# Optimization experiments

Measured on AMD Instinct MI355X. Metric: run time of the kernel, lower is better.

Reference implementation:

```python
import jax, jax.numpy as jnp
from jax import lax
import numpy as np

T, B, I, H, F, KEEP = 1000, 512, 64, 64, 128, 5
ALPHA = 20.0 / 100.0  # dt / tau


def setup_inputs() -> dict:
    key = jax.random.key(0)
    ks = jax.random.split(key, 9)
    s = 1.0 / np.sqrt(H)
    return {
        "x": jax.random.normal(ks[0], (T, B, I), jnp.float32),
        "h0": jnp.zeros((B, H), jnp.float32),
        "W_in": jax.random.normal(ks[1], (H, I), jnp.float32) * s,
        "b_in": jax.random.normal(ks[2], (H,), jnp.float32) * s,
        "W_hh": jax.random.normal(ks[3], (H, H), jnp.float32) * s,
        "b_hh": jax.random.normal(ks[4], (H,), jnp.float32) * s,
        "W1": jax.random.normal(ks[5], (F, KEEP * H), jnp.float32) / np.sqrt(KEEP * H),
        "b1": jax.random.normal(ks[6], (F,), jnp.float32) * 0.01,
        "W2": jax.random.normal(ks[7], (H, F), jnp.float32) / np.sqrt(F),
        "b2": jax.random.normal(ks[8], (H,), jnp.float32) * 0.01,
    }


def reference(x, h0, W_in, b_in, W_hh, b_hh, W1, b1, W2, b2):
    # CT-RNN with leaky integration; feedback via MLP on the last 5 hiddens
    # once 5 steps have accumulated. KC = 0.5*I, so the feedback mix is
    # h = 0.5*h_obs + 0.5*h_mlp.
    Tn, Bn, _ = x.shape
    Hn = h0.shape[1]
    buf0 = jnp.zeros((KEEP, Bn, Hn), x.dtype)  # oldest-first ring of hiddens

    def step(carry, inp):
        h, buf = carry
        xt, i = inp
        h_obs = jax.nn.relu(xt @ W_in.T + b_in + h @ W_hh.T + b_hh)
        h_obs = h * (1.0 - ALPHA) + h_obs * ALPHA
        # mlp feedback on concat of last 5 hiddens (oldest..newest) -> [B, 5H]
        mlp_in = buf.transpose(1, 0, 2).reshape(Bn, KEEP * Hn)
        h_mlp = jax.nn.relu(mlp_in @ W1.T + b1) @ W2.T + b2
        h_new = jnp.where(i >= KEEP, 0.5 * h_obs + 0.5 * h_mlp, h_obs)
        buf = jnp.concatenate([buf[1:], h_new[None]], axis=0)
        return (h_new, buf), h_new

    (hT, _), out = lax.scan(step, (h0, buf0), (x, jnp.arange(Tn)))
    return out, hT
```

## Files before the change

### kernel.cpp

```cpp
#include <hip/hip_runtime.h>

typedef short bf16x8 __attribute__((ext_vector_type(8)));
typedef float f32x4  __attribute__((ext_vector_type(4)));

#define TSTEPS 1000
#define BATCH  512
#define HID    64
#define INPD   64
#define FEAT   128
#define KEEP   5
#define KH     320
#define ALPHA  0.2f
#define BB     2
#define NBLK   (BATCH/BB)
#define NTHR   512

#define MFMA(a,b,c) __builtin_amdgcn_mfma_f32_16x16x32_bf16(a, b, c, 0, 0, 0)

template<int P> struct IC { static constexpr int v = P; };

__device__ __forceinline__ void barrier_fast() {
  asm volatile("s_waitcnt lgkmcnt(0)" ::: "memory");
  __builtin_amdgcn_s_barrier();
  asm volatile("" ::: "memory");
}

__device__ __forceinline__ f32x4 fold2(f32x4 v) {
  f32x4 r;
  r.x = v.x + __shfl_xor(v.x, 2);
  r.y = v.y + __shfl_xor(v.y, 2);
  r.z = v.z + __shfl_xor(v.z, 2);
  r.w = v.w + __shfl_xor(v.w, 2);
  return r;
}

__device__ __forceinline__ void pack4(float x0, float x1, float x2, float x3,
                                      unsigned &h0, unsigned &h1,
                                      unsigned &l0, unsigned &l1) {
  unsigned a0 = __float_as_uint(x0), a1 = __float_as_uint(x1);
  unsigned a2 = __float_as_uint(x2), a3 = __float_as_uint(x3);
  h0 = __builtin_amdgcn_perm(a1, a0, 0x07060302u);
  h1 = __builtin_amdgcn_perm(a3, a2, 0x07060302u);
  float r0 = x0 - __uint_as_float(a0 & 0xFFFF0000u);
  float r1 = x1 - __uint_as_float(a1 & 0xFFFF0000u);
  float r2 = x2 - __uint_as_float(a2 & 0xFFFF0000u);
  float r3 = x3 - __uint_as_float(a3 & 0xFFFF0000u);
  asm("v_cvt_pk_bf16_f32 %0, %1, %2" : "=v"(l0) : "v"(r0), "v"(r1));
  asm("v_cvt_pk_bf16_f32 %0, %1, %2" : "=v"(l1) : "v"(r2), "v"(r3));
}

__device__ __forceinline__ void pack_frag(float4 v0, float4 v1, bf16x8 &hi, bf16x8 &lo) {
  int4 h4, l4;
  pack4(v0.x, v0.y, v0.z, v0.w, (unsigned&)h4.x, (unsigned&)h4.y, (unsigned&)l4.x, (unsigned&)l4.y);
  pack4(v1.x, v1.y, v1.z, v1.w, (unsigned&)h4.z, (unsigned&)h4.w, (unsigned&)l4.z, (unsigned&)l4.w);
  hi = __builtin_bit_cast(bf16x8, h4);
  lo = __builtin_bit_cast(bf16x8, l4);
}

__device__ __forceinline__ void load_wfrag(const float* p, bf16x8 &hi, bf16x8 &lo) {
  float4 v0 = *(const float4*)p;
  float4 v1 = *(const float4*)(p + 4);
  pack_frag(v0, v1, hi, lo);
}

__global__ __launch_bounds__(NTHR, 2) void seq_kernel(
    const float* __restrict__ x,    float* __restrict__ io,
    const float* __restrict__ h0g,
    const float* __restrict__ W_in, const float* __restrict__ b_in,
    const float* __restrict__ W_hh, const float* __restrict__ b_hh,
    const float* __restrict__ W1,   const float* __restrict__ b1,
    const float* __restrict__ W2,   const float* __restrict__ b2) {

  __shared__ __align__(16) short B1lds[1024];
  __shared__ __align__(16) short a_s[512];
  __shared__ __align__(16) float xin_s[2][128];

  const int tid  = threadIdx.x;
  const int w    = tid >> 6;
  const int lane = tid & 63;
  const int q15  = lane & 15;
  const int g    = lane >> 4;
  const int b0   = blockIdx.x * BB;
  const bool gA  = (w < 4);
  const int r0c  = 16*(w & 3) + 4*g;
  const int f0   = 16*w + 4*g;
  const int c01  = q15 & 1;

  const int aWH = (w>>1)*128 + (2*(w&1) + (g>>1))*32 + q15*8 + 4*(g&1);
  const int aRD = g*32 + (q15 & 3)*8;
  const int bWH = ((w&3)>>1)*512 + ((2*(w&3) + (g>>1)) & 3)*128 + q15*8 + 4*(g&1);
  const int bRD = g*128 + q15*8;

  const f32x4 vz = {0.f, 0.f, 0.f, 0.f};
  const bf16x8 z8 = {0,0,0,0,0,0,0,0};

  bf16x8 w1h[10], w1l[10];
#pragma unroll
  for (int jt = 0; jt < 10; ++jt)
    load_wfrag(W1 + (size_t)(16*w + q15)*KH + jt*32 + 8*g, w1h[jt], w1l[jt]);

  bf16x8 wxh[6], wxl[6];
#pragma unroll
  for (int i = 0; i < 6; ++i) { wxh[i] = z8; wxl[i] = z8; }
  f32x4 biasv = vz, b2r = vz;
  f32x4 b1r = *(const f32x4*)(b1 + f0);
  if (gA) {
#pragma unroll
    for (int kt = 0; kt < 2; ++kt)
      load_wfrag(W_hh + (size_t)(16*w + q15)*HID + kt*32 + 8*g, wxh[kt], wxl[kt]);
#pragma unroll
    for (int kt = 0; kt < 4; ++kt)
      load_wfrag(W2 + (size_t)(16*w + q15)*FEAT + kt*32 + 8*g, wxh[2+kt], wxl[2+kt]);
    b2r = *(const f32x4*)(b2 + r0c);
  } else {
#pragma unroll
    for (int kt = 0; kt < 2; ++kt)
      load_wfrag(W_in + (size_t)(16*(w-4) + q15)*INPD + kt*32 + 8*g, wxh[kt], wxl[kt]);
    biasv = *(const f32x4*)(b_in + r0c) + *(const f32x4*)(b_hh + r0c);
  }

  for (int i = tid; i < 512; i += NTHR) ((unsigned*)B1lds)[i] = 0u;
  __syncthreads();

  f32x4 hprev = vz;
  float4 xc0, xc1, xc2, xc3;
  if (gA) {
    if (q15 < 2) {
      hprev = *(const f32x4*)(h0g + (size_t)(b0 + q15)*HID + r0c);
      unsigned n0, n1, n2, n3;
      pack4(hprev.x, hprev.y, hprev.z, hprev.w, n0, n1, n2, n3);
      *(uint2*)&B1lds[bWH]      = make_uint2(n0, n1);
      *(uint2*)&B1lds[bWH + 16] = make_uint2(n2, n3);
    }
  } else {
    const float* xp = x + (size_t)(b0 + c01)*INPD + 8*g;
    float4 v0 = *(const float4*)xp;        float4 v1 = *(const float4*)(xp + 4);
    float4 v2 = *(const float4*)(xp + 32); float4 v3 = *(const float4*)(xp + 36);
    bf16x8 th0, tl0, th1, tl1;
    pack_frag(v0, v1, th0, tl0);
    pack_frag(v2, v3, th1, tl1);
    bf16x8 f0b = (q15 & 2) ? tl0 : th0;
    bf16x8 f1b = (q15 & 2) ? tl1 : th1;
    f32x4 aHx = vz, aLx = vz;
    aHx = MFMA(wxh[0], f0b, aHx); aHx = MFMA(wxh[1], f1b, aHx);
    aLx = MFMA(wxl[0], f0b, aLx); aLx = MFMA(wxl[1], f1b, aLx);
    f32x4 xi = fold2(aHx + aLx) + biasv;
    if (q15 < 2) *(f32x4*)&xin_s[0][q15*64 + r0c] = xi;
    const float* xq = x + (size_t)1*BATCH*INPD + (size_t)(b0 + c01)*INPD + 8*g;
    xc0 = *(const float4*)xq;        xc1 = *(const float4*)(xq + 4);
    xc2 = *(const float4*)(xq + 32); xc3 = *(const float4*)(xq + 36);
  }

  bf16x8 rb[KEEP][2];
#pragma unroll
  for (int s = 0; s < KEEP; ++s) { rb[s][0] = z8; rb[s][1] = z8; }

  f32x4 aH = vz, aL = vz;
  __syncthreads();

  int t5 = 0;
  auto step = [&](auto pc) {
    constexpr int ph = decltype(pc)::v;
    constexpr int sN = (ph + 4) % 5;
    const int t = t5 + ph;

    rb[sN][0] = *(const bf16x8*)&B1lds[bRD];
    rb[sN][1] = *(const bf16x8*)&B1lds[bRD + 512];

    aH = MFMA(w1h[8], rb[sN][0], aH);
    aL = MFMA(w1l[8], rb[sN][0], aL);
    aH = MFMA(w1h[9], rb[sN][1], aH);
    aL = MFMA(w1l[9], rb[sN][1], aL);
    {
      f32x4 apre = fold2(aH + aL) + b1r;
      f32x4 av = __builtin_elementwise_max(apre, vz);
      unsigned p0, p1, p2, p3;
      pack4(av.x, av.y, av.z, av.w, p0, p1, p2, p3);
      if (q15 < 2) {
        *(uint2*)&a_s[aWH]      = make_uint2(p0, p1);
        *(uint2*)&a_s[aWH + 16] = make_uint2(p2, p3);
      }
    }
    barrier_fast();

    f32x4 nH = vz, nL = vz;
    if (gA) {
      bf16x8 af0 = *(const bf16x8*)&a_s[aRD +   0];
      bf16x8 af1 = *(const bf16x8*)&a_s[aRD + 128];
      bf16x8 af2 = *(const bf16x8*)&a_s[aRD + 256];
      bf16x8 af3 = *(const bf16x8*)&a_s[aRD + 384];
      f32x4 xinv = *(const f32x4*)&xin_s[t & 1][(q15 & 1)*64 + r0c];
#pragma unroll
      for (int r = 0; r < 4; ++r) {
        const int s = (ph + 1 + r) % 5;
        nH = MFMA(w1h[2*r],   rb[s][0], nH);
        nH = MFMA(w1h[2*r+1], rb[s][1], nH);
        nL = MFMA(w1l[2*r],   rb[s][0], nL);
        nL = MFMA(w1l[2*r+1], rb[s][1], nL);
      }
      f32x4 rH = vz, rL = vz;
      rH = MFMA(wxh[0], rb[sN][0], rH); rH = MFMA(wxh[1], rb[sN][1], rH);
      rL = MFMA(wxl[0], rb[sN][0], rL); rL = MFMA(wxl[1], rb[sN][1], rL);
      f32x4 mH = vz, mL = vz;
      mH = MFMA(wxh[2], af0, mH); mL = MFMA(wxl[2], af0, mL);
      mH = MFMA(wxh[3], af1, mH); mL = MFMA(wxl[3], af1, mL);
      mH = MFMA(wxh[4], af2, mH); mL = MFMA(wxl[4], af2, mL);
      mH = MFMA(wxh[5], af3, mH); mL = MFMA(wxl[5], af3, mL);
      f32x4 pre = fold2(rH + rL) + xinv;
      f32x4 rl_ = __builtin_elementwise_max(pre, vz);
      f32x4 hobs = hprev * (1.f - ALPHA) + rl_ * ALPHA;
      f32x4 hm = fold2(mH + mL) + b2r;
      f32x4 hn = (t >= KEEP) ? (hobs + hm) * 0.5f : hobs;
      if (q15 < 2) {
        *(f32x4*)(io + (size_t)t*BATCH*HID + (size_t)(b0 + q15)*HID + r0c) = hn;
        if (t == TSTEPS-1)
          *(f32x4*)(io + (size_t)TSTEPS*BATCH*HID + (size_t)(b0 + q15)*HID + r0c) = hn;
        unsigned n0, n1, n2, n3;
        pack4(hn.x, hn.y, hn.z, hn.w, n0, n1, n2, n3);
        *(uint2*)&B1lds[bWH]      = make_uint2(n0, n1);
        *(uint2*)&B1lds[bWH + 16] = make_uint2(n2, n3);
      }
      hprev = hn;
    } else {
      float4 xn0, xn1, xn2, xn3;
      {
        int tn = t + 2; if (tn > TSTEPS-1) tn = TSTEPS-1;
        const float* xp = x + (size_t)tn*BATCH*INPD + (size_t)(b0 + c01)*INPD + 8*g;
        xn0 = *(const float4*)xp;        xn1 = *(const float4*)(xp + 4);
        xn2 = *(const float4*)(xp + 32); xn3 = *(const float4*)(xp + 36);
      }
#pragma unroll
      for (int r = 0; r < 4; ++r) {
        const int s = (ph + 1 + r) % 5;
        nH = MFMA(w1h[2*r],   rb[s][0], nH);
        nH = MFMA(w1h[2*r+1], rb[s][1], nH);
        nL = MFMA(w1l[2*r],   rb[s][0], nL);
        nL = MFMA(w1l[2*r+1], rb[s][1], nL);
      }
      bf16x8 th0, tl0, th1, tl1;
      pack_frag(xc0, xc1, th0, tl0);
      pack_frag(xc2, xc3, th1, tl1);
      bf16x8 f0b = (q15 & 2) ? tl0 : th0;
      bf16x8 f1b = (q15 & 2) ? tl1 : th1;
      f32x4 xH = vz, xL = vz;
      xH = MFMA(wxh[0], f0b, xH); xH = MFMA(wxh[1], f1b, xH);
      xL = MFMA(wxl[0], f0b, xL); xL = MFMA(wxl[1], f1b, xL);
      f32x4 xi = fold2(xH + xL) + biasv;
      if (q15 < 2) *(f32x4*)&xin_s[(t + 1) & 1][q15*64 + r0c] = xi;
      xc0 = xn0; xc1 = xn1; xc2 = xn2; xc3 = xn3;
    }
    aH = nH; aL = nL;
    barrier_fast();
  };

  for (t5 = 0; t5 < TSTEPS; t5 += 5) {
    step(IC<0>{});
    step(IC<1>{});
    step(IC<2>{});
    step(IC<3>{});
    step(IC<4>{});
  }
}

extern "C" void kernel_launch(void* const* d_in, const int* in_sizes, int n_in,
                              void* d_out, int out_size, void* d_ws, size_t ws_size,
                              hipStream_t stream) {
  (void)in_sizes; (void)n_in; (void)out_size; (void)d_ws; (void)ws_size;
  const float* x    = (const float*)d_in[0];
  const float* h0   = (const float*)d_in[1];
  const float* W_in = (const float*)d_in[2];
  const float* b_in = (const float*)d_in[3];
  const float* W_hh = (const float*)d_in[4];
  const float* b_hh = (const float*)d_in[5];
  const float* W1   = (const float*)d_in[6];
  const float* b1   = (const float*)d_in[7];
  const float* W2   = (const float*)d_in[8];
  const float* b2   = (const float*)d_in[9];
  float* out = (float*)d_out;

  seq_kernel<<<NBLK, NTHR, 0, stream>>>(x, out, h0, W_in, b_in, W_hh, b_hh, W1, b1, W2, b2);
}
```

Baseline: 974.3 us.

## Reschedule per-step MFMA chains to shorten the recurrent critical path

Reorders the MLP first-layer accumulation so the contributions of older hidden states are computed before the barrier, off the critical path. The recurrent W_hh product and the leaky update now run before the barrier. Long dependent MFMA chains are split into independent partial accumulators to cut serial latency. The xor-2 lane shuffle in fold2 is replaced with a DPP quad permute. This adds register pressure and changes the floating-point summation order slightly.

```diff
diff --git a/kernel.cpp b/kernel.cpp
--- a/kernel.cpp
+++ b/kernel.cpp
@@ -25,12 +25,16 @@
   asm volatile("" ::: "memory");
 }
 
+__device__ __forceinline__ float qx2(float v) {
+  return __uint_as_float((unsigned)__builtin_amdgcn_update_dpp(
+      0, (int)__float_as_uint(v), 0x4E , 0xF, 0xF, true));
+}
 __device__ __forceinline__ f32x4 fold2(f32x4 v) {
   f32x4 r;
-  r.x = v.x + __shfl_xor(v.x, 2);
-  r.y = v.y + __shfl_xor(v.y, 2);
-  r.z = v.z + __shfl_xor(v.z, 2);
-  r.w = v.w + __shfl_xor(v.w, 2);
+  r.x = v.x + qx2(v.x);
+  r.y = v.y + qx2(v.y);
+  r.z = v.z + qx2(v.z);
+  r.w = v.w + qx2(v.w);
   return r;
 }
 
@@ -155,24 +159,29 @@
 #pragma unroll
   for (int s = 0; s < KEEP; ++s) { rb[s][0] = z8; rb[s][1] = z8; }
 
-  f32x4 aH = vz, aL = vz;
+  f32x4 accH = vz, accL = vz;
   __syncthreads();
 
   int t5 = 0;
   auto step = [&](auto pc) {
     constexpr int ph = decltype(pc)::v;
     constexpr int sN = (ph + 4) % 5;
+    constexpr int s3 = (ph + 3) % 5;
+    constexpr int s2 = (ph + 2) % 5;
+    constexpr int s1 = (ph + 1) % 5;
     const int t = t5 + ph;
 
     rb[sN][0] = *(const bf16x8*)&B1lds[bRD];
     rb[sN][1] = *(const bf16x8*)&B1lds[bRD + 512];
-
-    aH = MFMA(w1h[8], rb[sN][0], aH);
-    aL = MFMA(w1l[8], rb[sN][0], aL);
-    aH = MFMA(w1h[9], rb[sN][1], aH);
-    aL = MFMA(w1l[9], rb[sN][1], aL);
+    f32x4 xinv = vz;
+    if (gA) xinv = *(const f32x4*)&xin_s[t & 1][(q15 & 1)*64 + r0c];
+
+    f32x4 tH = MFMA(w1h[9], rb[sN][1], vz);
+    f32x4 tL = MFMA(w1l[9], rb[sN][1], vz);
+    accH = MFMA(w1h[8], rb[sN][0], accH);
+    accL = MFMA(w1l[8], rb[sN][0], accL);
     {
-      f32x4 apre = fold2(aH + aL) + b1r;
+      f32x4 apre = fold2((accH + tH) + (accL + tL)) + b1r;
       f32x4 av = __builtin_elementwise_max(apre, vz);
       unsigned p0, p1, p2, p3;
       pack4(av.x, av.y, av.z, av.w, p0, p1, p2, p3);
@@ -181,35 +190,50 @@
         *(uint2*)&a_s[aWH + 16] = make_uint2(p2, p3);
       }
     }
+
+    f32x4 hobs = vz;
+    if (gA) {
+      f32x4 rH = MFMA(wxh[0], rb[sN][0], vz);
+      f32x4 rL = MFMA(wxl[0], rb[sN][0], vz);
+      rH = MFMA(wxh[1], rb[sN][1], rH);
+      rL = MFMA(wxl[1], rb[sN][1], rL);
+      f32x4 pre = fold2(rH + rL) + xinv;
+      f32x4 rl_ = __builtin_elementwise_max(pre, vz);
+      hobs = hprev * (1.f - ALPHA) + rl_ * ALPHA;
+    }
+
+    accH = MFMA(w1h[4], rb[s3][0], vz);
+    accL = MFMA(w1l[4], rb[s3][0], vz);
+    accH = MFMA(w1h[5], rb[s3][1], accH);
+    accL = MFMA(w1l[5], rb[s3][1], accL);
+    accH = MFMA(w1h[6], rb[sN][0], accH);
+    accL = MFMA(w1l[6], rb[sN][0], accL);
+    accH = MFMA(w1h[7], rb[sN][1], accH);
+    accL = MFMA(w1l[7], rb[sN][1], accL);
     barrier_fast();
 
-    f32x4 nH = vz, nL = vz;
     if (gA) {
       bf16x8 af0 = *(const bf16x8*)&a_s[aRD +   0];
       bf16x8 af1 = *(const bf16x8*)&a_s[aRD + 128];
       bf16x8 af2 = *(const bf16x8*)&a_s[aRD + 256];
       bf16x8 af3 = *(const bf16x8*)&a_s[aRD + 384];
-      f32x4 xinv = *(const f32x4*)&xin_s[t & 1][(q15 & 1)*64 + r0c];
-#pragma unroll
-      for (int r = 0; r < 4; ++r) {
-        const int s = (ph + 1 + r) % 5;
-        nH = MFMA(w1h[2*r],   rb[s][0], nH);
-        nH = MFMA(w1h[2*r+1], rb[s][1], nH);
-        nL = MFMA(w1l[2*r],   rb[s][0], nL);
-        nL = MFMA(w1l[2*r+1], rb[s][1], nL);
-      }
-      f32x4 rH = vz, rL = vz;
-      rH = MFMA(wxh[0], rb[sN][0], rH); rH = MFMA(wxh[1], rb[sN][1], rH);
-      rL = MFMA(wxl[0], rb[sN][0], rL); rL = MFMA(wxl[1], rb[sN][1], rL);
-      f32x4 mH = vz, mL = vz;
-      mH = MFMA(wxh[2], af0, mH); mL = MFMA(wxl[2], af0, mL);
-      mH = MFMA(wxh[3], af1, mH); mL = MFMA(wxl[3], af1, mL);
-      mH = MFMA(wxh[4], af2, mH); mL = MFMA(wxl[4], af2, mL);
-      mH = MFMA(wxh[5], af3, mH); mL = MFMA(wxl[5], af3, mL);
-      f32x4 pre = fold2(rH + rL) + xinv;
-      f32x4 rl_ = __builtin_elementwise_max(pre, vz);
-      f32x4 hobs = hprev * (1.f - ALPHA) + rl_ * ALPHA;
-      f32x4 hm = fold2(mH + mL) + b2r;
+      accH = MFMA(w1h[0], rb[s1][0], accH);
+      accL = MFMA(w1l[0], rb[s1][0], accL);
+      accH = MFMA(w1h[1], rb[s1][1], accH);
+      accL = MFMA(w1l[1], rb[s1][1], accL);
+      accH = MFMA(w1h[2], rb[s2][0], accH);
+      accL = MFMA(w1l[2], rb[s2][0], accL);
+      accH = MFMA(w1h[3], rb[s2][1], accH);
+      accL = MFMA(w1l[3], rb[s2][1], accL);
+      f32x4 mH0 = MFMA(wxh[2], af0, vz);
+      f32x4 mL0 = MFMA(wxl[2], af0, vz);
+      f32x4 mH1 = MFMA(wxh[4], af2, vz);
+      f32x4 mL1 = MFMA(wxl[4], af2, vz);
+      mH0 = MFMA(wxh[3], af1, mH0);
+      mL0 = MFMA(wxl[3], af1, mL0);
+      mH1 = MFMA(wxh[5], af3, mH1);
+      mL1 = MFMA(wxl[5], af3, mL1);
+      f32x4 hm = fold2((mH0 + mH1) + (mL0 + mL1)) + b2r;
       f32x4 hn = (t >= KEEP) ? (hobs + hm) * 0.5f : hobs;
       if (q15 < 2) {
         *(f32x4*)(io + (size_t)t*BATCH*HID + (size_t)(b0 + q15)*HID + r0c) = hn;
@@ -229,27 +253,27 @@
         xn0 = *(const float4*)xp;        xn1 = *(const float4*)(xp + 4);
         xn2 = *(const float4*)(xp + 32); xn3 = *(const float4*)(xp + 36);
       }
-#pragma unroll
-      for (int r = 0; r < 4; ++r) {
-        const int s = (ph + 1 + r) % 5;
-        nH = MFMA(w1h[2*r],   rb[s][0], nH);
-        nH = MFMA(w1h[2*r+1], rb[s][1], nH);
-        nL = MFMA(w1l[2*r],   rb[s][0], nL);
-        nL = MFMA(w1l[2*r+1], rb[s][1], nL);
-      }
+      accH = MFMA(w1h[0], rb[s1][0], accH);
+      accL = MFMA(w1l[0], rb[s1][0], accL);
+      accH = MFMA(w1h[1], rb[s1][1], accH);
+      accL = MFMA(w1l[1], rb[s1][1], accL);
+      accH = MFMA(w1h[2], rb[s2][0], accH);
+      accL = MFMA(w1l[2], rb[s2][0], accL);
+      accH = MFMA(w1h[3], rb[s2][1], accH);
+      accL = MFMA(w1l[3], rb[s2][1], accL);
       bf16x8 th0, tl0, th1, tl1;
       pack_frag(xc0, xc1, th0, tl0);
       pack_frag(xc2, xc3, th1, tl1);
       bf16x8 f0b = (q15 & 2) ? tl0 : th0;
       bf16x8 f1b = (q15 & 2) ? tl1 : th1;
-      f32x4 xH = vz, xL = vz;
-      xH = MFMA(wxh[0], f0b, xH); xH = MFMA(wxh[1], f1b, xH);
-      xL = MFMA(wxl[0], f0b, xL); xL = MFMA(wxl[1], f1b, xL);
+      f32x4 xH = MFMA(wxh[0], f0b, vz);
+      f32x4 xL = MFMA(wxl[0], f0b, vz);
+      xH = MFMA(wxh[1], f1b, xH);
+      xL = MFMA(wxl[1], f1b, xL);
       f32x4 xi = fold2(xH + xL) + biasv;
       if (q15 < 2) *(f32x4*)&xin_s[(t + 1) & 1][q15*64 + r0c] = xi;
       xc0 = xn0; xc1 = xn1; xc2 = xn2; xc3 = xn3;
     }
-    aH = nH; aL = nL;
     barrier_fast();
   };
 
```

Result: slower. 1.004 ms (+3.0%).
